# Optimization experiments

Measured on AMD Instinct MI355X. Metric: run time of the kernel, lower is better.

## Reference

```python
import jax, jax.numpy as jnp
import numpy as np

N, CIN, T, HF, WF = 1, 64, 8, 96, 96
C = 256
H, W = HF // 4, WF // 4
K = 27  # 3 dilations (1,3,5) x 3x3 kernel taps

# kernel-tap offsets, ordered: dilation-major, then row-major 3x3 (matches cat order)
_OFFS = np.array([(oy * d, ox * d) for d in (1, 3, 5) for oy in (-1, 0, 1) for ox in (-1, 0, 1)], dtype=np.float32)


def setup_inputs() -> dict:
    key = jax.random.key(0)
    ks = jax.random.split(key, 6)
    return {
        "input": jax.random.normal(ks[0], (N, CIN, T, HF, WF), jnp.float32),
        "flow": 2.0 * jax.random.normal(ks[1], (N, 2, T, H, W), jnp.float32),
        "w_node": 0.02 * jax.random.normal(ks[2], (C, CIN, 4, 4), jnp.float32),  # Conv3d(64,256,(1,4,4)) with unit time-kernel squeezed
        "b_node": jnp.zeros((C,), jnp.float32),
        "w_up": 0.02 * jax.random.normal(ks[3], (C, 64, 4, 4), jnp.float32),  # ConvTranspose3d(256,64,(1,4,4)) weight [in,out,kh,kw]
        "b_up": jnp.zeros((64,), jnp.float32),
        "w_out": 0.05 * jax.random.normal(ks[4], (64, 64), jnp.float32),  # 1x1x1 Conv3d(64,64)
        "b_out": jnp.zeros((64,), jnp.float32),
        "B": T,
    }


def _deform_sample(node, flow):
    # Deformable neighbor sampling for all 3 dilations at once.
    # node [N,C,T,H,W], flow [N,2,T,H,W] (y,x offsets) -> neighbour [N,C,T,H,W,K]
    n, c, t, h, w = node.shape
    off = jnp.asarray(_OFFS)  # [K,2]
    yy = jnp.arange(h, dtype=node.dtype)[:, None]   # [H,1]
    xx = jnp.arange(w, dtype=node.dtype)[None, :]   # [1,W]
    # sampling positions [N,T,K,H,W]
    py = (yy + off[:, 0][:, None, None]) + flow[:, 0][:, :, None]
    px = (xx + off[:, 1][:, None, None]) + flow[:, 1][:, :, None]
    y0 = jnp.floor(py)
    x0 = jnp.floor(px)
    ty = py - y0
    tx = px - x0
    y0 = y0.astype(jnp.int32)
    x0 = x0.astype(jnp.int32)
    nf = node.transpose(0, 2, 1, 3, 4).reshape(n, t, c, h * w)  # [N,T,C,HW]

    def gather(yi, xi):
        valid = ((yi >= 0) & (yi < h) & (xi >= 0) & (xi < w)).astype(node.dtype)
        idx = jnp.clip(yi, 0, h - 1) * w + jnp.clip(xi, 0, w - 1)  # [N,T,K,H,W]
        idx = jnp.broadcast_to(idx.reshape(n, t, 1, K * h * w), (n, t, c, K * h * w))
        v = jnp.take_along_axis(nf, idx, axis=-1).reshape(n, t, c, K, h, w)
        return v * valid[:, :, None]  # zero-pad outside

    samp = (gather(y0, x0) * ((1 - ty) * (1 - tx))[:, :, None]
            + gather(y0, x0 + 1) * ((1 - ty) * tx)[:, :, None]
            + gather(y0 + 1, x0) * (ty * (1 - tx))[:, :, None]
            + gather(y0 + 1, x0 + 1) * (ty * tx)[:, :, None])  # [N,T,C,K,H,W]
    return samp.transpose(0, 2, 1, 4, 5, 3)  # [N,C,T,H,W,K]


def reference(input, flow, w_node, b_node, w_up, b_up, w_out, b_out, B):
    n, cin, t, hf, wf = input.shape
    h, w = hf // 4, wf // 4
    # layer_node: kernel==stride (1,4,4) conv == non-overlapping 4x4 patch projection
    xr = input.reshape(n, cin, t, h, 4, w, 4)
    node = jnp.einsum('ncthawb,ocab->nothw', xr, w_node) + b_node[None, :, None, None, None]  # [N,C,T,H,W]
    c = node.shape[1]

    neighbour = _deform_sample(node, flow)  # [N,C,T,H,W,27] == cat(dcn1,dcn2,dcn3)

    nhw = n * h * w
    node_b = node.transpose(0, 3, 4, 2, 1).reshape(nhw, t, c)                      # [NHW,B,C]
    nb_a = neighbour.transpose(0, 3, 4, 1, 2, 5).reshape(nhw, c, t * K)            # [NHW,C,B*27]
    A = node_b @ nb_a                                                              # [NHW,B,B*27]
    nb_b = neighbour.transpose(0, 3, 4, 2, 5, 1).reshape(nhw, t * K, c)            # [NHW,B*27,C]
    out = (1.0 / 216.0) * (A @ nb_b)                                               # [NHW,B,C]
    out = out.reshape(n, h, w, t, c).transpose(0, 4, 3, 1, 2)                      # [N,C,T,H,W]

    # layer_out: ConvTranspose (k==stride, pad 0) == per-pixel 4x4 block expansion, then 1x1x1 conv
    up = jnp.einsum('ncthw,coab->nothawb', out, w_up).reshape(n, 64, t, 4 * h, 4 * w)
    up = up + b_up[None, :, None, None, None]
    return jnp.einsum('ncthw,oc->nothw', up, w_out) + b_out[None, :, None, None, None]
```

## Files before the change

### kernel.cpp

```cpp
#include <hip/hip_runtime.h>


typedef unsigned short ushort_t;
typedef ushort_t ushort8 __attribute__((ext_vector_type(8)));
typedef __bf16 bf16x8 __attribute__((ext_vector_type(8)));
typedef __bf16 bf16x2 __attribute__((ext_vector_type(2)));
typedef float f32x4 __attribute__((ext_vector_type(4)));
typedef unsigned int uint4v __attribute__((ext_vector_type(4)));

#define NSTR 264
#define ASTR 40

#define OFF_NH0   0
#define OFF_NH1   16896
#define OFF_AS    33792
#define OFF_BASES 38912
#define OFF_WTS   42496
#define ATTN_LDS  46080

__device__ __forceinline__ ushort_t f2bf(float f) {
    __bf16 h = (__bf16)f;
    return __builtin_bit_cast(ushort_t, h);
}
__device__ __forceinline__ float blo(unsigned u) { return __uint_as_float(u << 16); }
__device__ __forceinline__ float bhi(unsigned u) { return __uint_as_float(u & 0xffff0000u); }
__device__ __forceinline__ unsigned pk2(float a, float b) {
    bf16x2 v = { (__bf16)a, (__bf16)b };
    return __builtin_bit_cast(unsigned, v);
}
__device__ __forceinline__ void gld_lds16(const void* g, void* l) {
    __builtin_amdgcn_global_load_lds(
        (const __attribute__((address_space(1))) unsigned*)g,
        (__attribute__((address_space(3))) unsigned*)l, 16, 0, 0);
}

__global__ __launch_bounds__(256) void k_prep(
    const float* __restrict__ w_node, const float* __restrict__ w_up,
    const float* __restrict__ w_out, const float* __restrict__ b_up,
    const float* __restrict__ b_out,
    ushort_t* __restrict__ w_node_perm, ushort_t* __restrict__ Wf_perm,
    float* __restrict__ bias_tot)
{
    __shared__ float wout_s[4096];
    int tid = threadIdx.x;
    for (int i = tid; i < 4096; i += 256) wout_s[i] = w_out[i];
    __syncthreads();
    int gid = blockIdx.x * 256 + tid;
    #pragma unroll
    for (int r = 0; r < 4; ++r) {
        int e = gid + r * 65536;
        {
            int k = e & 1023, n = e >> 10;
            w_node_perm[(((k >> 3) << 8) + n) * 8 + (k & 7)] = f2bf(w_node[n * 1024 + k]);
        }
        {
            int n = e & 1023, k = e >> 10;
            int o = n >> 4, ab = n & 15;
            const float* wo = wout_s + o * 64;
            const float* wu = w_up + (k << 10) + ab;
            float s0 = 0.f, s1 = 0.f, s2 = 0.f, s3 = 0.f;
            #pragma unroll 4
            for (int c = 0; c < 64; c += 4) {
                s0 += wo[c]     * wu[c << 4];
                s1 += wo[c + 1] * wu[(c + 1) << 4];
                s2 += wo[c + 2] * wu[(c + 2) << 4];
                s3 += wo[c + 3] * wu[(c + 3) << 4];
            }
            Wf_perm[(((k >> 3) << 10) + n) * 8 + (k & 7)] = f2bf((s0 + s1) + (s2 + s3));
        }
    }
    if (blockIdx.x == 0 && tid < 64) {
        float s = b_out[tid];
        const float* wo = wout_s + tid * 64;
        #pragma unroll 8
        for (int c = 0; c < 64; ++c) s += wo[c] * b_up[c];
        bias_tot[tid] = s;
    }
}

template<int FINAL>
__global__ __launch_bounds__(256) void k_gemm(
    const float* __restrict__ input, const ushort_t* __restrict__ a_bf,
    const ushort_t* __restrict__ w_perm, const float* __restrict__ bias,
    ushort_t* __restrict__ node_bf, float* __restrict__ dout)
{
    constexpr int KS = FINAL ? 4 : 16;
    constexpr int N  = FINAL ? 1024 : 256;
    constexpr int BN = FINAL ? 128 : 64;
    constexpr int NI = FINAL ? 2 : 1;
    constexpr int RB = BN / 32;
    __shared__ __align__(16) ushort_t A_lds[2][2048];
    __shared__ __align__(16) ushort_t B_lds[2][BN * 64];
    int tid  = threadIdx.x;
    int lane = tid & 63, wid = tid >> 6;
    int g = lane >> 4, r16 = lane & 15;
    int m0 = blockIdx.x * 32, n0 = blockIdx.y * BN;

    const float*   inpA = nullptr;
    const ushort_t* finA = nullptr;
    int ldsA_slot;
    if constexpr (!FINAL) {
        int mA = tid & 31, kcA = tid >> 5;
        int m = m0 + mA;
        int t = m / 576, hw = m % 576, hh = hw / 24, ww = hw % 24;
        inpA = input + (size_t)(kcA >> 1) * 73728 + t * 9216 + hh * 384 + ww * 4 + (kcA & 1) * 192;
        ldsA_slot = (kcA * 32 + mA) * 8;
    } else {
        int m = m0 + (tid >> 3), q = tid & 7;
        finA = a_bf + m * 256 + ((q ^ (m & 7)) * 8);
        ldsA_slot = tid * 8;
    }

    f32x4 acc[2][NI];
    #pragma unroll
    for (int i = 0; i < 2; ++i)
        #pragma unroll
        for (int j = 0; j < NI; ++j) acc[i][j] = (f32x4){0.f, 0.f, 0.f, 0.f};

    float4 fa, fb;
    #pragma unroll
    for (int r = 0; r < RB; ++r) {
        int s = r * 256 + tid;
        int kc = s / BN, n = s % BN;
        gld_lds16(w_perm + (size_t)((kc * N + n0 + n) * 8), &B_lds[0][s * 8]);
    }
    if constexpr (FINAL) {
        gld_lds16(finA, &A_lds[0][ldsA_slot]);
    } else {
        fa = *(const float4*)(inpA);
        fb = *(const float4*)(inpA + 96);
        uint4v p;
        p.x = pk2(fa.x, fa.y); p.y = pk2(fa.z, fa.w);
        p.z = pk2(fb.x, fb.y); p.w = pk2(fb.z, fb.w);
        *(uint4v*)&A_lds[0][ldsA_slot] = p;
    }
    __syncthreads();

    for (int kb = 0; kb < KS; ++kb) {
        int cur = kb & 1, nxt = cur ^ 1;
        bool more = (kb + 1 < KS);
        if (more) {
            #pragma unroll
            for (int r = 0; r < RB; ++r) {
                int s = r * 256 + tid;
                int kc = s / BN, n = s % BN;
                gld_lds16(w_perm + (size_t)((((kb + 1) * 8 + kc) * N + n0 + n) * 8),
                          &B_lds[nxt][s * 8]);
            }
            if constexpr (FINAL) {
                gld_lds16(finA + (kb + 1) * 64, &A_lds[nxt][ldsA_slot]);
            } else {
                fa = *(const float4*)(inpA + (size_t)(kb + 1) * 294912);
                fb = *(const float4*)(inpA + (size_t)(kb + 1) * 294912 + 96);
            }
        }
        bf16x8 af[2][2], bfr[NI][2];
        #pragma unroll
        for (int mi = 0; mi < 2; ++mi)
            #pragma unroll
            for (int ks = 0; ks < 2; ++ks) {
                int idx;
                if constexpr (!FINAL) idx = ((ks * 4 + g) * 32 + mi * 16 + r16) * 8;
                else                  idx = (mi * 16 + r16) * 64 + (((ks * 4 + g) ^ (r16 & 7)) * 8);
                af[mi][ks] = __builtin_bit_cast(bf16x8, *(const ushort8*)&A_lds[cur][idx]);
            }
        #pragma unroll
        for (int ni = 0; ni < NI; ++ni)
            #pragma unroll
            for (int ks = 0; ks < 2; ++ks) {
                int idx = ((ks * 4 + g) * BN + wid * (BN / 4) + ni * 16 + r16) * 8;
                bfr[ni][ks] = __builtin_bit_cast(bf16x8, *(const ushort8*)&B_lds[cur][idx]);
            }
        #pragma unroll
        for (int mi = 0; mi < 2; ++mi)
            #pragma unroll
            for (int ni = 0; ni < NI; ++ni)
                #pragma unroll
                for (int ks = 0; ks < 2; ++ks)
                    acc[mi][ni] = __builtin_amdgcn_mfma_f32_16x16x32_bf16(
                        af[mi][ks], bfr[ni][ks], acc[mi][ni], 0, 0, 0);
        if constexpr (!FINAL) {
            if (more) {
                uint4v p;
                p.x = pk2(fa.x, fa.y); p.y = pk2(fa.z, fa.w);
                p.z = pk2(fb.x, fb.y); p.w = pk2(fb.z, fb.w);
                *(uint4v*)&A_lds[nxt][ldsA_slot] = p;
            }
        }
        __syncthreads();
    }

    if constexpr (!FINAL) {
        int n = n0 + wid * 16 + r16;
        float bv = bias[n];
        #pragma unroll
        for (int mi = 0; mi < 2; ++mi)
            #pragma unroll
            for (int rr = 0; rr < 4; ++rr) {
                int m = m0 + mi * 16 + 4 * g + rr;
                node_bf[(size_t)m * 256 + n] = f2bf(acc[mi][0][rr] + bv);
            }
    } else {
        constexpr int EPS = 132;
        float* ep = (float*)&B_lds[0][0];
        #pragma unroll
        for (int ni = 0; ni < NI; ++ni) {
            int n = wid * 32 + ni * 16 + r16;
            #pragma unroll
            for (int mi = 0; mi < 2; ++mi)
                #pragma unroll
                for (int rr = 0; rr < 4; ++rr)
                    ep[(mi * 16 + 4 * g + rr) * EPS + n] = acc[mi][ni][rr];
        }
        __syncthreads();
        #pragma unroll
        for (int r = 0; r < 4; ++r) {
            int task = r * 256 + tid;
            int mloc = task & 31, nb4 = task >> 5;
            float4 v = *(const float4*)&ep[mloc * EPS + nb4 * 4];
            int n = n0 + nb4 * 4;
            int o = n >> 4, aa = (n >> 2) & 3;
            float bv = bias[o];
            int m = m0 + mloc;
            int t = m / 576, hw = m % 576, hh = hw / 24, ww = hw % 24;
            float* dst = dout + ((size_t)(o * 8 + t) * 96 + hh * 4 + aa) * 96 + ww * 4;
            *(float4*)dst = make_float4(v.x + bv, v.y + bv, v.z + bv, v.w + bv);
        }
    }
}

__device__ __forceinline__ void combine8(
    uint4v t0, uint4v t1, uint4v t2, uint4v t3,
    uint4v t4, uint4v t5, uint4v t6, uint4v t7,
    float4 wA, float4 wB, ushort_t* __restrict__ nh, int jl, int c0)
{
    uint4v outA, outB;
    #pragma unroll
    for (int p = 0; p < 4; ++p) {
        unsigned a0 = t0[p], a1 = t1[p], a2 = t2[p], a3 = t3[p];
        unsigned b0 = t4[p], b1 = t5[p], b2 = t6[p], b3 = t7[p];
        float aL = wA.x * blo(a0) + wA.y * blo(a1) + wA.z * blo(a2) + wA.w * blo(a3);
        float aH = wA.x * bhi(a0) + wA.y * bhi(a1) + wA.z * bhi(a2) + wA.w * bhi(a3);
        float bL = wB.x * blo(b0) + wB.y * blo(b1) + wB.z * blo(b2) + wB.w * blo(b3);
        float bH = wB.x * bhi(b0) + wB.y * bhi(b1) + wB.z * bhi(b2) + wB.w * bhi(b3);
        outA[p] = pk2(aL, aH);
        outB[p] = pk2(bL, bH);
    }
    *(uint4v*)(nh + jl * NSTR + c0)       = outA;
    *(uint4v*)(nh + (jl + 1) * NSTR + c0) = outB;
}

__global__ __launch_bounds__(256) void k_attn(
    const ushort_t* __restrict__ node_bf, const float* __restrict__ flow,
    ushort_t* __restrict__ out_bf)
{
    extern __shared__ char smem[];
    int*      bases = (int*)(smem + OFF_BASES);
    float*    wts   = (float*)(smem + OFF_WTS);

    int tid  = threadIdx.x;
    int pos  = blockIdx.x;
    int h    = pos / 24, w = pos % 24;
    int lane = tid & 63, wid = tid >> 6;
    int g    = lane >> 4, r16 = lane & 15;
    ushort_t* A_w = (ushort_t*)(smem + OFF_AS) + wid * 640;

    if (tid < 224) {
        int j = tid;
        float w00 = 0, w01 = 0, w10 = 0, w11 = 0;
        int b00 = 0, b01 = 0, b10 = 0, b11 = 0;
        if (j < 216) {
            int tt = j / 27, kk = j - tt * 27;
            int d  = 2 * (kk / 9) + 1;
            int oy = (kk / 3) % 3 - 1, ox = kk % 3 - 1;
            float fy = flow[tt * 576 + pos];
            float fx = flow[4608 + tt * 576 + pos];
            float py = (float)(h + oy * d) + fy;
            float px = (float)(w + ox * d) + fx;
            float fy0 = floorf(py), fx0 = floorf(px);
            int y0 = (int)fy0, x0 = (int)fx0;
            float ty = py - fy0, tx = px - fx0;
            int y0c = min(max(y0, 0), 23), y1c = min(max(y0 + 1, 0), 23);
            int x0c = min(max(x0, 0), 23), x1c = min(max(x0 + 1, 0), 23);
            float vy0 = (y0 >= 0 && y0 < 24) ? 1.f : 0.f;
            float vy1 = (y0 >= -1 && y0 < 23) ? 1.f : 0.f;
            float vx0 = (x0 >= 0 && x0 < 24) ? 1.f : 0.f;
            float vx1 = (x0 >= -1 && x0 < 23) ? 1.f : 0.f;
            w00 = (1.f - ty) * (1.f - tx) * vy0 * vx0;
            w01 = (1.f - ty) * tx * vy0 * vx1;
            w10 = ty * (1.f - tx) * vy1 * vx0;
            w11 = ty * tx * vy1 * vx1;
            int base_t = tt * 576 * 256;
            b00 = base_t + (y0c * 24 + x0c) * 256;
            b01 = base_t + (y0c * 24 + x1c) * 256;
            b10 = base_t + (y1c * 24 + x0c) * 256;
            b11 = base_t + (y1c * 24 + x1c) * 256;
        }
        bases[j * 4 + 0] = b00; bases[j * 4 + 1] = b01;
        bases[j * 4 + 2] = b10; bases[j * 4 + 3] = b11;
        wts[j * 4 + 0] = w00; wts[j * 4 + 1] = w01;
        wts[j * 4 + 2] = w10; wts[j * 4 + 3] = w11;
    }

    bf16x8 nbf[8];
    {
        int t = r16;
        const ushort_t* src = node_bf + ((size_t)(t & 7) * 576 + pos) * 256 + g * 8;
        ushort8 uz = {};
        #pragma unroll
        for (int s = 0; s < 8; ++s) {
            ushort8 uu = *(const ushort8*)(src + s * 32);
            nbf[s] = __builtin_bit_cast(bf16x8, (t < 8) ? uu : uz);
        }
    }

    f32x4 oacc[4];
    #pragma unroll
    for (int i = 0; i < 4; ++i) oacc[i] = (f32x4){0.f, 0.f, 0.f, 0.f};

    __syncthreads();

    const int jp2  = (tid >> 4) * 2;
    const int c0lo = (tid & 15) * 16;
    const int c0hi = c0lo + 8;

    uint4v rA0, rA1, rA2, rA3, rA4, rA5, rA6, rA7;
    uint4v rB0, rB1, rB2, rB3, rB4, rB5, rB6, rB7;

    #define PREFETCH(TILE) do {                                   \
        int jA_ = (TILE) * 32 + jp2;                              \
        int4 bsA_ = *(const int4*)&bases[jA_ * 4];                \
        int4 bsB_ = *(const int4*)&bases[jA_ * 4 + 4];            \
        rA0 = *(const uint4v*)(node_bf + bsA_.x + c0lo);          \
        rA1 = *(const uint4v*)(node_bf + bsA_.y + c0lo);          \
        rA2 = *(const uint4v*)(node_bf + bsA_.z + c0lo);          \
        rA3 = *(const uint4v*)(node_bf + bsA_.w + c0lo);          \
        rA4 = *(const uint4v*)(node_bf + bsB_.x + c0lo);          \
        rA5 = *(const uint4v*)(node_bf + bsB_.y + c0lo);          \
        rA6 = *(const uint4v*)(node_bf + bsB_.z + c0lo);          \
        rA7 = *(const uint4v*)(node_bf + bsB_.w + c0lo);          \
        rB0 = *(const uint4v*)(node_bf + bsA_.x + c0hi);          \
        rB1 = *(const uint4v*)(node_bf + bsA_.y + c0hi);          \
        rB2 = *(const uint4v*)(node_bf + bsA_.z + c0hi);          \
        rB3 = *(const uint4v*)(node_bf + bsA_.w + c0hi);          \
        rB4 = *(const uint4v*)(node_bf + bsB_.x + c0hi);          \
        rB5 = *(const uint4v*)(node_bf + bsB_.y + c0hi);          \
        rB6 = *(const uint4v*)(node_bf + bsB_.z + c0hi);          \
        rB7 = *(const uint4v*)(node_bf + bsB_.w + c0hi);          \
    } while (0)

    #define COMBINE(TILE, nh) do {                                              \
        int jC_ = (TILE) * 32 + jp2;                                            \
        float4 wA_ = *(const float4*)&wts[jC_ * 4];                             \
        float4 wB_ = *(const float4*)&wts[jC_ * 4 + 4];                         \
        combine8(rA0, rA1, rA2, rA3, rA4, rA5, rA6, rA7, wA_, wB_, nh, jp2, c0lo); \
        combine8(rB0, rB1, rB2, rB3, rB4, rB5, rB6, rB7, wA_, wB_, nh, jp2, c0hi); \
    } while (0)

    PREFETCH(0);
    COMBINE(0, (ushort_t*)(smem + OFF_NH0));
    PREFETCH(1);
    __syncthreads();

    for (int k = 0; k < 7; ++k) {
        int cur = k & 1;
        ushort_t* nh = (ushort_t*)(smem + (cur ? OFF_NH1 : OFF_NH0));

        f32x4 aacc0 = {0.f, 0.f, 0.f, 0.f};
        f32x4 aacc1 = {0.f, 0.f, 0.f, 0.f};
        #pragma unroll
        for (int s = 0; s < 8; ++s) {
            const ushort_t* bp0 = nh + r16 * NSTR + s * 32 + g * 8;
            bf16x8 bf0 = __builtin_bit_cast(bf16x8, *(const ushort8*)bp0);
            aacc0 = __builtin_amdgcn_mfma_f32_16x16x32_bf16(nbf[s], bf0, aacc0, 0, 0, 0);
            const ushort_t* bp1 = nh + (16 + r16) * NSTR + s * 32 + g * 8;
            bf16x8 bf1 = __builtin_bit_cast(bf16x8, *(const ushort8*)bp1);
            aacc1 = __builtin_amdgcn_mfma_f32_16x16x32_bf16(nbf[s], bf1, aacc1, 0, 0, 0);
        }
        {
            const float sc = 1.f / 216.f;
            #pragma unroll
            for (int rr = 0; rr < 4; ++rr) {
                A_w[(4 * g + rr) * ASTR + r16]      = f2bf(aacc0[rr] * sc);
                A_w[(4 * g + rr) * ASTR + 16 + r16] = f2bf(aacc1[rr] * sc);
            }
        }
        bf16x8 afrag = __builtin_bit_cast(bf16x8, *(const ushort8*)(A_w + r16 * ASTR + g * 8));

        #pragma unroll
        for (int i = 0; i < 4; ++i) {
            int cc = wid * 64 + i * 16 + r16;
            ushort8 bv;
            #pragma unroll
            for (int e = 0; e < 8; ++e) bv[e] = nh[(g * 8 + e) * NSTR + cc];
            bf16x8 bfrag = __builtin_bit_cast(bf16x8, bv);
            oacc[i] = __builtin_amdgcn_mfma_f32_16x16x32_bf16(afrag, bfrag, oacc[i], 0, 0, 0);
        }

        if (k < 6) {
            ushort_t* nh2 = (ushort_t*)(smem + (cur ? OFF_NH0 : OFF_NH1));
            COMBINE(k + 1, nh2);
            if (k <= 4) PREFETCH(k + 2);
        }
        __syncthreads();
    }
    #undef PREFETCH
    #undef COMBINE

    if (g < 2) {
        #pragma unroll
        for (int i = 0; i < 4; ++i) {
            int c = wid * 64 + i * 16 + r16;
            #pragma unroll
            for (int rr = 0; rr < 4; ++rr) {
                int t = 4 * g + rr;
                out_bf[((size_t)t * 576 + pos) * 256 + c] = f2bf(oacc[i][rr]);
            }
        }
    }
}

extern "C" void kernel_launch(void* const* d_in, const int* in_sizes, int n_in,
                              void* d_out, int out_size, void* d_ws, size_t ws_size,
                              hipStream_t stream) {
    (void)in_sizes; (void)n_in; (void)out_size; (void)ws_size;
    const float* input  = (const float*)d_in[0];
    const float* flow   = (const float*)d_in[1];
    const float* w_node = (const float*)d_in[2];
    const float* b_node = (const float*)d_in[3];
    const float* w_up   = (const float*)d_in[4];
    const float* b_up   = (const float*)d_in[5];
    const float* w_out  = (const float*)d_in[6];
    const float* b_out  = (const float*)d_in[7];
    float* dout = (float*)d_out;

    char* wsb = (char*)d_ws;
    ushort_t* node_bf = (ushort_t*)wsb;
    ushort_t* out_bf  = (ushort_t*)(wsb + 2359296);
    ushort_t* w_np    = (ushort_t*)(wsb + 4718592);
    ushort_t* wf_p    = (ushort_t*)(wsb + 5242880);
    float*    bias_t  = (float*)(wsb + 5767168);

    k_prep<<<256, 256, 0, stream>>>(w_node, w_up, w_out, b_up, b_out, w_np, wf_p, bias_t);
    k_gemm<0><<<dim3(144, 4), 256, 0, stream>>>(input, nullptr, w_np, b_node, node_bf, nullptr);
    hipFuncSetAttribute(reinterpret_cast<const void*>(k_attn),
                        hipFuncAttributeMaxDynamicSharedMemorySize, ATTN_LDS);
    k_attn<<<576, 256, ATTN_LDS, stream>>>(node_bf, flow, out_bf);
    k_gemm<1><<<dim3(144, 8), 256, 0, stream>>>(nullptr, out_bf, wf_p, bias_t, nullptr, dout);
}
```

Baseline: 65.11 us.

## Split attention block into two warp groups ping-ponging gather-combine and MFMA compute

Doubles the k_attn block to 512 threads, organised as two 256-thread groups that each own one neighbour buffer. The groups alternate phases, so one gathers and combines a tile of deformable samples while the other runs the two-stage MFMA on its tile. At the end the partial output accumulators are reduced through LDS. This is meant to overlap global gather latency with matrix compute inside one block. In exchange it adds more LDS, a cross-group reduction and tighter register limits from launch_bounds(512,4).

New measurement: 88.19 us. +35.4%, slower.

```diff
diff --git a/kernel.cpp b/kernel.cpp
--- a/kernel.cpp
+++ b/kernel.cpp
@@ -14,9 +14,9 @@
 #define OFF_NH0   0
 #define OFF_NH1   16896
 #define OFF_AS    33792
-#define OFF_BASES 38912
-#define OFF_WTS   42496
-#define ATTN_LDS  46080
+#define OFF_BASES 44032
+#define OFF_WTS   48128
+#define ATTN_LDS  52224
 
 __device__ __forceinline__ ushort_t f2bf(float f) {
     __bf16 h = (__bf16)f;
@@ -250,22 +250,26 @@
     *(uint4v*)(nh + (jl + 1) * NSTR + c0) = outB;
 }
 
-__global__ __launch_bounds__(256) void k_attn(
+__global__ __launch_bounds__(512, 4) void k_attn(
     const ushort_t* __restrict__ node_bf, const float* __restrict__ flow,
     ushort_t* __restrict__ out_bf)
 {
     extern __shared__ char smem[];
-    int*      bases = (int*)(smem + OFF_BASES);
-    float*    wts   = (float*)(smem + OFF_WTS);
+    int*   bases = (int*)(smem + OFF_BASES);
+    float* wts   = (float*)(smem + OFF_WTS);
 
     int tid  = threadIdx.x;
     int pos  = blockIdx.x;
     int h    = pos / 24, w = pos % 24;
     int lane = tid & 63, wid = tid >> 6;
+    int grp  = wid >> 2;
+    int wid4 = wid & 3;
     int g    = lane >> 4, r16 = lane & 15;
-    ushort_t* A_w = (ushort_t*)(smem + OFF_AS) + wid * 640;
-
-    if (tid < 224) {
+    int t256 = tid & 255;
+    ushort_t* A_w  = (ushort_t*)(smem + OFF_AS) + wid * 640;
+    ushort_t* myNH = (ushort_t*)(smem + (grp ? OFF_NH1 : OFF_NH0));
+
+    if (tid < 256) {
         int j = tid;
         float w00 = 0, w01 = 0, w10 = 0, w11 = 0;
         int b00 = 0, b01 = 0, b10 = 0, b11 = 0;
@@ -320,101 +324,105 @@
 
     __syncthreads();
 
-    const int jp2  = (tid >> 4) * 2;
-    const int c0lo = (tid & 15) * 16;
+    const int jp2  = (t256 >> 4) * 2;
+    const int c0lo = (t256 & 15) * 16;
     const int c0hi = c0lo + 8;
 
-    uint4v rA0, rA1, rA2, rA3, rA4, rA5, rA6, rA7;
-    uint4v rB0, rB1, rB2, rB3, rB4, rB5, rB6, rB7;
-
-    #define PREFETCH(TILE) do {                                   \
+    uint4v pL0, pL1, pL2, pL3, pL4, pL5, pL6, pL7;
+
+    #define PREFETCH_LO(TILE) do {                                \
         int jA_ = (TILE) * 32 + jp2;                              \
         int4 bsA_ = *(const int4*)&bases[jA_ * 4];                \
         int4 bsB_ = *(const int4*)&bases[jA_ * 4 + 4];            \
-        rA0 = *(const uint4v*)(node_bf + bsA_.x + c0lo);          \
-        rA1 = *(const uint4v*)(node_bf + bsA_.y + c0lo);          \
-        rA2 = *(const uint4v*)(node_bf + bsA_.z + c0lo);          \
-        rA3 = *(const uint4v*)(node_bf + bsA_.w + c0lo);          \
-        rA4 = *(const uint4v*)(node_bf + bsB_.x + c0lo);          \
-        rA5 = *(const uint4v*)(node_bf + bsB_.y + c0lo);          \
-        rA6 = *(const uint4v*)(node_bf + bsB_.z + c0lo);          \
-        rA7 = *(const uint4v*)(node_bf + bsB_.w + c0lo);          \
-        rB0 = *(const uint4v*)(node_bf + bsA_.x + c0hi);          \
-        rB1 = *(const uint4v*)(node_bf + bsA_.y + c0hi);          \
-        rB2 = *(const uint4v*)(node_bf + bsA_.z + c0hi);          \
-        rB3 = *(const uint4v*)(node_bf + bsA_.w + c0hi);          \
-        rB4 = *(const uint4v*)(node_bf + bsB_.x + c0hi);          \
-        rB5 = *(const uint4v*)(node_bf + bsB_.y + c0hi);          \
-        rB6 = *(const uint4v*)(node_bf + bsB_.z + c0hi);          \
-        rB7 = *(const uint4v*)(node_bf + bsB_.w + c0hi);          \
+        pL0 = *(const uint4v*)(node_bf + bsA_.x + c0lo);          \
+        pL1 = *(const uint4v*)(node_bf + bsA_.y + c0lo);          \
+        pL2 = *(const uint4v*)(node_bf + bsA_.z + c0lo);          \
+        pL3 = *(const uint4v*)(node_bf + bsA_.w + c0lo);          \
+        pL4 = *(const uint4v*)(node_bf + bsB_.x + c0lo);          \
+        pL5 = *(const uint4v*)(node_bf + bsB_.y + c0lo);          \
+        pL6 = *(const uint4v*)(node_bf + bsB_.z + c0lo);          \
+        pL7 = *(const uint4v*)(node_bf + bsB_.w + c0lo);          \
     } while (0)
 
-    #define COMBINE(TILE, nh) do {                                              \
-        int jC_ = (TILE) * 32 + jp2;                                            \
-        float4 wA_ = *(const float4*)&wts[jC_ * 4];                             \
-        float4 wB_ = *(const float4*)&wts[jC_ * 4 + 4];                         \
-        combine8(rA0, rA1, rA2, rA3, rA4, rA5, rA6, rA7, wA_, wB_, nh, jp2, c0lo); \
-        combine8(rB0, rB1, rB2, rB3, rB4, rB5, rB6, rB7, wA_, wB_, nh, jp2, c0hi); \
-    } while (0)
-
-    PREFETCH(0);
-    COMBINE(0, (ushort_t*)(smem + OFF_NH0));
-    PREFETCH(1);
+    PREFETCH_LO(grp);
+
+    for (int p = 0; p < 9; ++p) {
+        bool doComb = (grp == 0) ? (((p & 1) == 0) && p < 8) : ((p & 1) == 1);
+        bool doComp = (grp == 0) ? ((p & 1) == 1) : (((p & 1) == 0) && p >= 2);
+
+        if (doComb) {
+            int ct = p;
+            int jA = ct * 32 + jp2;
+            int4 bsA = *(const int4*)&bases[jA * 4];
+            int4 bsB = *(const int4*)&bases[jA * 4 + 4];
+            float4 wA = *(const float4*)&wts[jA * 4];
+            float4 wB = *(const float4*)&wts[jA * 4 + 4];
+            uint4v h0 = *(const uint4v*)(node_bf + bsA.x + c0hi);
+            uint4v h1 = *(const uint4v*)(node_bf + bsA.y + c0hi);
+            uint4v h2 = *(const uint4v*)(node_bf + bsA.z + c0hi);
+            uint4v h3 = *(const uint4v*)(node_bf + bsA.w + c0hi);
+            uint4v h4 = *(const uint4v*)(node_bf + bsB.x + c0hi);
+            uint4v h5 = *(const uint4v*)(node_bf + bsB.y + c0hi);
+            uint4v h6 = *(const uint4v*)(node_bf + bsB.z + c0hi);
+            uint4v h7 = *(const uint4v*)(node_bf + bsB.w + c0hi);
+            combine8(pL0, pL1, pL2, pL3, pL4, pL5, pL6, pL7, wA, wB, myNH, jp2, c0lo);
+            if (ct + 2 < 8) PREFETCH_LO(ct + 2);
+            combine8(h0, h1, h2, h3, h4, h5, h6, h7, wA, wB, myNH, jp2, c0hi);
+        }
+
+        if (doComp) {
+            f32x4 aacc0 = {0.f, 0.f, 0.f, 0.f};
+            f32x4 aacc1 = {0.f, 0.f, 0.f, 0.f};
+            #pragma unroll
+            for (int s = 0; s < 8; ++s) {
+                const ushort_t* bp0 = myNH + r16 * NSTR + s * 32 + g * 8;
+                bf16x8 bf0 = __builtin_bit_cast(bf16x8, *(const ushort8*)bp0);
+                aacc0 = __builtin_amdgcn_mfma_f32_16x16x32_bf16(nbf[s], bf0, aacc0, 0, 0, 0);
+                const ushort_t* bp1 = myNH + (16 + r16) * NSTR + s * 32 + g * 8;
+                bf16x8 bf1 = __builtin_bit_cast(bf16x8, *(const ushort8*)bp1);
+                aacc1 = __builtin_amdgcn_mfma_f32_16x16x32_bf16(nbf[s], bf1, aacc1, 0, 0, 0);
+            }
+            {
+                const float sc = 1.f / 216.f;
+                #pragma unroll
+                for (int rr = 0; rr < 4; ++rr) {
+                    A_w[(4 * g + rr) * ASTR + r16]      = f2bf(aacc0[rr] * sc);
+                    A_w[(4 * g + rr) * ASTR + 16 + r16] = f2bf(aacc1[rr] * sc);
+                }
+            }
+            bf16x8 afrag = __builtin_bit_cast(bf16x8, *(const ushort8*)(A_w + r16 * ASTR + g * 8));
+            #pragma unroll
+            for (int i = 0; i < 4; ++i) {
+                int cc = wid4 * 64 + i * 16 + r16;
+                ushort8 bv;
+                #pragma unroll
+                for (int e = 0; e < 8; ++e) bv[e] = myNH[(g * 8 + e) * NSTR + cc];
+                bf16x8 bfrag = __builtin_bit_cast(bf16x8, bv);
+                oacc[i] = __builtin_amdgcn_mfma_f32_16x16x32_bf16(afrag, bfrag, oacc[i], 0, 0, 0);
+            }
+        }
+        __syncthreads();
+    }
+    #undef PREFETCH_LO
+
+    float* red = (float*)smem;
+    if (grp == 1 && g < 2) {
+        #pragma unroll
+        for (int i = 0; i < 4; ++i)
+            #pragma unroll
+            for (int rr = 0; rr < 4; ++rr)
+                red[((wid4 * 4 + i) * 32 + g * 16 + r16) * 4 + rr] = oacc[i][rr];
+    }
     __syncthreads();
-
-    for (int k = 0; k < 7; ++k) {
-        int cur = k & 1;
-        ushort_t* nh = (ushort_t*)(smem + (cur ? OFF_NH1 : OFF_NH0));
-
-        f32x4 aacc0 = {0.f, 0.f, 0.f, 0.f};
-        f32x4 aacc1 = {0.f, 0.f, 0.f, 0.f};
-        #pragma unroll
-        for (int s = 0; s < 8; ++s) {
-            const ushort_t* bp0 = nh + r16 * NSTR + s * 32 + g * 8;
-            bf16x8 bf0 = __builtin_bit_cast(bf16x8, *(const ushort8*)bp0);
-            aacc0 = __builtin_amdgcn_mfma_f32_16x16x32_bf16(nbf[s], bf0, aacc0, 0, 0, 0);
-            const ushort_t* bp1 = nh + (16 + r16) * NSTR + s * 32 + g * 8;
-            bf16x8 bf1 = __builtin_bit_cast(bf16x8, *(const ushort8*)bp1);
-            aacc1 = __builtin_amdgcn_mfma_f32_16x16x32_bf16(nbf[s], bf1, aacc1, 0, 0, 0);
-        }
-        {
-            const float sc = 1.f / 216.f;
-            #pragma unroll
-            for (int rr = 0; rr < 4; ++rr) {
-                A_w[(4 * g + rr) * ASTR + r16]      = f2bf(aacc0[rr] * sc);
-                A_w[(4 * g + rr) * ASTR + 16 + r16] = f2bf(aacc1[rr] * sc);
-            }
-        }
-        bf16x8 afrag = __builtin_bit_cast(bf16x8, *(const ushort8*)(A_w + r16 * ASTR + g * 8));
-
+    if (grp == 0 && g < 2) {
         #pragma unroll
         for (int i = 0; i < 4; ++i) {
-            int cc = wid * 64 + i * 16 + r16;
-            ushort8 bv;
-            #pragma unroll
-            for (int e = 0; e < 8; ++e) bv[e] = nh[(g * 8 + e) * NSTR + cc];
-            bf16x8 bfrag = __builtin_bit_cast(bf16x8, bv);
-            oacc[i] = __builtin_amdgcn_mfma_f32_16x16x32_bf16(afrag, bfrag, oacc[i], 0, 0, 0);
-        }
-
-        if (k < 6) {
-            ushort_t* nh2 = (ushort_t*)(smem + (cur ? OFF_NH0 : OFF_NH1));
-            COMBINE(k + 1, nh2);
-            if (k <= 4) PREFETCH(k + 2);
-        }
-        __syncthreads();
-    }
-    #undef PREFETCH
-    #undef COMBINE
-
-    if (g < 2) {
-        #pragma unroll
-        for (int i = 0; i < 4; ++i) {
-            int c = wid * 64 + i * 16 + r16;
+            int c = wid4 * 64 + i * 16 + r16;
             #pragma unroll
             for (int rr = 0; rr < 4; ++rr) {
                 int t = 4 * g + rr;
-                out_bf[((size_t)t * 576 + pos) * 256 + c] = f2bf(oacc[i][rr]);
+                float v = oacc[i][rr] + red[((wid4 * 4 + i) * 32 + g * 16 + r16) * 4 + rr];
+                out_bf[((size_t)t * 576 + pos) * 256 + c] = f2bf(v);
             }
         }
     }
@@ -445,6 +453,6 @@
     k_gemm<0><<<dim3(144, 4), 256, 0, stream>>>(input, nullptr, w_np, b_node, node_bf, nullptr);
     hipFuncSetAttribute(reinterpret_cast<const void*>(k_attn),
                         hipFuncAttributeMaxDynamicSharedMemorySize, ATTN_LDS);
-    k_attn<<<576, 256, ATTN_LDS, stream>>>(node_bf, flow, out_bf);
+    k_attn<<<576, 512, ATTN_LDS, stream>>>(node_bf, flow, out_bf);
     k_gemm<1><<<dim3(144, 8), 256, 0, stream>>>(nullptr, out_bf, wf_p, bias_t, nullptr, dout);
 }
```

## Add transposed swizzled LDS copy of neighbour tile for vectorised MFMA B-fragment loads

Applied to the files above, without the earlier changes.

The combine step now also writes a channel-major, XOR-swizzled transposed copy of each bilinear-sampled neighbour tile into new double-buffered LDS regions. The second MFMA can then load its B fragment as a single 16-byte LDS read instead of eight strided 2-byte reads. The combine for the next tile is moved ahead of the second GEMM so it overlaps with it. The prep kernel stages w_up slices in LDS and pads w_out rows to avoid bank conflicts. In exchange, LDS use grows from about 46 KB to 79 KB per block, which may reduce occupancy, and each combine does extra scattered LDS writes.

After: 97.72 us. 1.5x slower.

```diff
diff --git a/kernel.cpp b/kernel.cpp
--- a/kernel.cpp
+++ b/kernel.cpp
@@ -8,15 +8,18 @@
 typedef float f32x4 __attribute__((ext_vector_type(4)));
 typedef unsigned int uint4v __attribute__((ext_vector_type(4)));
 
-#define NSTR 264
+#define NSTR 268
+#define TSTR 32
 #define ASTR 40
 
 #define OFF_NH0   0
-#define OFF_NH1   16896
-#define OFF_AS    33792
-#define OFF_BASES 38912
-#define OFF_WTS   42496
-#define ATTN_LDS  46080
+#define OFF_NH1   17152
+#define OFF_NT0   34304
+#define OFF_NT1   50688
+#define OFF_AS    67072
+#define OFF_BASES 72192
+#define OFF_WTS   75776
+#define ATTN_LDS  79360
 
 __device__ __forceinline__ ushort_t f2bf(float f) {
     __bf16 h = (__bf16)f;
@@ -26,6 +29,10 @@
 __device__ __forceinline__ float bhi(unsigned u) { return __uint_as_float(u & 0xffff0000u); }
 __device__ __forceinline__ unsigned pk2(float a, float b) {
     bf16x2 v = { (__bf16)a, (__bf16)b };
+    return __builtin_bit_cast(unsigned, v);
+}
+__device__ __forceinline__ unsigned pk2h(__bf16 a, __bf16 b) {
+    bf16x2 v = { a, b };
     return __builtin_bit_cast(unsigned, v);
 }
 __device__ __forceinline__ void gld_lds16(const void* g, void* l) {
@@ -41,23 +48,29 @@
     ushort_t* __restrict__ w_node_perm, ushort_t* __restrict__ Wf_perm,
     float* __restrict__ bias_tot)
 {
-    __shared__ float wout_s[4096];
+    __shared__ float wout_s[64 * 66];
+    __shared__ float wu_s[1024];
     int tid = threadIdx.x;
-    for (int i = tid; i < 4096; i += 256) wout_s[i] = w_out[i];
-    __syncthreads();
+    for (int i = tid; i < 4096; i += 256)
+        wout_s[(i >> 6) * 66 + (i & 63)] = w_out[i];
     int gid = blockIdx.x * 256 + tid;
-    #pragma unroll
+    int kbase = blockIdx.x >> 2;
+    #pragma unroll 1
     for (int r = 0; r < 4; ++r) {
         int e = gid + r * 65536;
         {
             int k = e & 1023, n = e >> 10;
             w_node_perm[(((k >> 3) << 8) + n) * 8 + (k & 7)] = f2bf(w_node[n * 1024 + k]);
         }
+        int kk = kbase + r * 64;
+        __syncthreads();
+        *(float4*)&wu_s[tid * 4] = *(const float4*)&w_up[kk * 1024 + tid * 4];
+        __syncthreads();
         {
-            int n = e & 1023, k = e >> 10;
+            int n = e & 1023;
             int o = n >> 4, ab = n & 15;
-            const float* wo = wout_s + o * 64;
-            const float* wu = w_up + (k << 10) + ab;
+            const float* wo = wout_s + o * 66;
+            const float* wu = wu_s + ab;
             float s0 = 0.f, s1 = 0.f, s2 = 0.f, s3 = 0.f;
             #pragma unroll 4
             for (int c = 0; c < 64; c += 4) {
@@ -66,12 +79,12 @@
                 s2 += wo[c + 2] * wu[(c + 2) << 4];
                 s3 += wo[c + 3] * wu[(c + 3) << 4];
             }
-            Wf_perm[(((k >> 3) << 10) + n) * 8 + (k & 7)] = f2bf((s0 + s1) + (s2 + s3));
+            Wf_perm[(((kk >> 3) << 10) + n) * 8 + (kk & 7)] = f2bf((s0 + s1) + (s2 + s3));
         }
     }
     if (blockIdx.x == 0 && tid < 64) {
         float s = b_out[tid];
-        const float* wo = wout_s + tid * 64;
+        const float* wo = wout_s + tid * 66;
         #pragma unroll 8
         for (int c = 0; c < 64; ++c) s += wo[c] * b_up[c];
         bias_tot[tid] = s;
@@ -232,9 +245,11 @@
 __device__ __forceinline__ void combine8(
     uint4v t0, uint4v t1, uint4v t2, uint4v t3,
     uint4v t4, uint4v t5, uint4v t6, uint4v t7,
-    float4 wA, float4 wB, ushort_t* __restrict__ nh, int jl, int c0)
+    float4 wA, float4 wB, ushort_t* __restrict__ nh, ushort_t* __restrict__ nt,
+    int jl, int c0)
 {
     uint4v outA, outB;
+    int dsw = ((jl >> 1) ^ (((c0 >> 4) & 3) << 2)) * 2;
     #pragma unroll
     for (int p = 0; p < 4; ++p) {
         unsigned a0 = t0[p], a1 = t1[p], a2 = t2[p], a3 = t3[p];
@@ -243,8 +258,12 @@
         float aH = wA.x * bhi(a0) + wA.y * bhi(a1) + wA.z * bhi(a2) + wA.w * bhi(a3);
         float bL = wB.x * blo(b0) + wB.y * blo(b1) + wB.z * blo(b2) + wB.w * blo(b3);
         float bH = wB.x * bhi(b0) + wB.y * bhi(b1) + wB.z * bhi(b2) + wB.w * bhi(b3);
-        outA[p] = pk2(aL, aH);
-        outB[p] = pk2(bL, bH);
+        __bf16 cAL = (__bf16)aL, cAH = (__bf16)aH;
+        __bf16 cBL = (__bf16)bL, cBH = (__bf16)bH;
+        outA[p] = pk2h(cAL, cAH);
+        outB[p] = pk2h(cBL, cBH);
+        *(unsigned*)(nt + (c0 + 2 * p) * TSTR + dsw)     = pk2h(cAL, cBL);
+        *(unsigned*)(nt + (c0 + 2 * p + 1) * TSTR + dsw) = pk2h(cAH, cBH);
     }
     *(uint4v*)(nh + jl * NSTR + c0)       = outA;
     *(uint4v*)(nh + (jl + 1) * NSTR + c0) = outB;
@@ -255,8 +274,8 @@
     ushort_t* __restrict__ out_bf)
 {
     extern __shared__ char smem[];
-    int*      bases = (int*)(smem + OFF_BASES);
-    float*    wts   = (float*)(smem + OFF_WTS);
+    int*   bases = (int*)(smem + OFF_BASES);
+    float* wts   = (float*)(smem + OFF_WTS);
 
     int tid  = threadIdx.x;
     int pos  = blockIdx.x;
@@ -349,22 +368,23 @@
         rB7 = *(const uint4v*)(node_bf + bsB_.w + c0hi);          \
     } while (0)
 
-    #define COMBINE(TILE, nh) do {                                              \
+    #define COMBINE(TILE, nh, nt) do {                                          \
         int jC_ = (TILE) * 32 + jp2;                                            \
         float4 wA_ = *(const float4*)&wts[jC_ * 4];                             \
         float4 wB_ = *(const float4*)&wts[jC_ * 4 + 4];                         \
-        combine8(rA0, rA1, rA2, rA3, rA4, rA5, rA6, rA7, wA_, wB_, nh, jp2, c0lo); \
-        combine8(rB0, rB1, rB2, rB3, rB4, rB5, rB6, rB7, wA_, wB_, nh, jp2, c0hi); \
+        combine8(rA0, rA1, rA2, rA3, rA4, rA5, rA6, rA7, wA_, wB_, nh, nt, jp2, c0lo); \
+        combine8(rB0, rB1, rB2, rB3, rB4, rB5, rB6, rB7, wA_, wB_, nh, nt, jp2, c0hi); \
     } while (0)
 
     PREFETCH(0);
-    COMBINE(0, (ushort_t*)(smem + OFF_NH0));
+    COMBINE(0, (ushort_t*)(smem + OFF_NH0), (ushort_t*)(smem + OFF_NT0));
     PREFETCH(1);
     __syncthreads();
 
     for (int k = 0; k < 7; ++k) {
         int cur = k & 1;
         ushort_t* nh = (ushort_t*)(smem + (cur ? OFF_NH1 : OFF_NH0));
+        ushort_t* nt = (ushort_t*)(smem + (cur ? OFF_NT1 : OFF_NT0));
 
         f32x4 aacc0 = {0.f, 0.f, 0.f, 0.f};
         f32x4 aacc1 = {0.f, 0.f, 0.f, 0.f};
@@ -385,23 +405,24 @@
                 A_w[(4 * g + rr) * ASTR + 16 + r16] = f2bf(aacc1[rr] * sc);
             }
         }
+
+        if (k < 6) {
+            ushort_t* nh2 = (ushort_t*)(smem + (cur ? OFF_NH0 : OFF_NH1));
+            ushort_t* nt2 = (ushort_t*)(smem + (cur ? OFF_NT0 : OFF_NT1));
+            COMBINE(k + 1, nh2, nt2);
+        }
+
         bf16x8 afrag = __builtin_bit_cast(bf16x8, *(const ushort8*)(A_w + r16 * ASTR + g * 8));
 
         #pragma unroll
         for (int i = 0; i < 4; ++i) {
             int cc = wid * 64 + i * 16 + r16;
-            ushort8 bv;
-            #pragma unroll
-            for (int e = 0; e < 8; ++e) bv[e] = nh[(g * 8 + e) * NSTR + cc];
-            bf16x8 bfrag = __builtin_bit_cast(bf16x8, bv);
+            const ushort_t* tp = nt + cc * TSTR + 8 * (g ^ i);
+            bf16x8 bfrag = __builtin_bit_cast(bf16x8, *(const ushort8*)tp);
             oacc[i] = __builtin_amdgcn_mfma_f32_16x16x32_bf16(afrag, bfrag, oacc[i], 0, 0, 0);
         }
 
-        if (k < 6) {
-            ushort_t* nh2 = (ushort_t*)(smem + (cur ? OFF_NH0 : OFF_NH1));
-            COMBINE(k + 1, nh2);
-            if (k <= 4) PREFETCH(k + 2);
-        }
+        if (k <= 4) PREFETCH(k + 2);
         __syncthreads();
     }
     #undef PREFETCH
```
